# Optimization experiments

Measured on AMD Instinct MI355X. Metric: run time of the kernel, lower is better.

Reference implementation:

```python
import jax, jax.numpy as jnp
import numpy as np

H = 1024      # hidden_size
NH = 16       # num heads
HD = H // NH  # head dim
B, S = 2, 2048


def setup_inputs() -> dict:
    key = jax.random.key(0)
    ks = jax.random.split(key, 10)
    s = 1.0 / np.sqrt(H)
    return {
        "hidden_states": jax.random.normal(ks[0], (B, S, H), dtype=jnp.float32),
        "attention_mask": jax.random.randint(ks[1], (B, S), 0, 2, dtype=jnp.int32),
        "Wq": jax.random.normal(ks[2], (H, H), dtype=jnp.float32) * s,
        "bq": jnp.zeros((H,), dtype=jnp.float32),
        "Wk": jax.random.normal(ks[3], (H, H), dtype=jnp.float32) * s,
        "bk": jnp.zeros((H,), dtype=jnp.float32),
        "Wv": jax.random.normal(ks[4], (H, H), dtype=jnp.float32) * s,
        "bv": jnp.zeros((H,), dtype=jnp.float32),
        "Wo": jax.random.normal(ks[5], (H, H), dtype=jnp.float32) * s,
        "bo": jnp.zeros((H,), dtype=jnp.float32),
    }


def _heads(x):
    # [B,S,H] -> [B,NH,S,HD]
    b, s, _ = x.shape
    return x.reshape(b, s, NH, HD).transpose(0, 2, 1, 3)


def reference(hidden_states, attention_mask, Wq, bq, Wk, bk, Wv, bv, Wo, bo):
    q = _heads(hidden_states @ Wq + bq)
    k = _heads(hidden_states @ Wk + bk)
    v = _heads(hidden_states @ Wv + bv)
    scores = jnp.einsum("bhqd,bhkd->bhqk", q, k) / jnp.sqrt(jnp.float32(HD))
    mask = attention_mask.astype(scores.dtype)[:, None, None, :]  # [B,1,1,S]
    scores = scores + mask * -10000.0
    probs = jax.nn.softmax(scores, axis=-1)  # dropout is identity in eval
    ctx = jnp.einsum("bhqk,bhkd->bhqd", probs, v)
    ctx = ctx.transpose(0, 2, 1, 3).reshape(hidden_states.shape[0], hidden_states.shape[1], H)
    return ctx @ Wo + bo
```

## Files before the change

### kernel.cpp

```cpp
#include <hip/hip_runtime.h>
#include <stdint.h>
#include <stddef.h>

#define S_LEN 2048
#define BATCH 2
#define HID 1024
#define NHEADS 16
#define HDIM 64

typedef __attribute__((ext_vector_type(8))) short short8;
typedef __attribute__((ext_vector_type(4))) short short4v;
typedef __attribute__((ext_vector_type(4))) float float4v;

#define MFMA32(a, b, c) __builtin_amdgcn_mfma_f32_16x16x32_bf16((a), (b), (c), 0, 0, 0)

#if __has_builtin(__builtin_amdgcn_mfma_f32_16x16x16_bf16)
#define MFMA16(a, b, c) __builtin_amdgcn_mfma_f32_16x16x16_bf16((a), (b), (c), 0, 0, 0)
#elif __has_builtin(__builtin_amdgcn_mfma_f32_16x16x16bf16_1k)
#define MFMA16(a, b, c) __builtin_amdgcn_mfma_f32_16x16x16bf16_1k((a), (b), (c), 0, 0, 0)
#else
static __device__ __forceinline__ float4v mfma16_asm(short4v a, short4v b, float4v c) {
  asm volatile("v_mfma_f32_16x16x16_bf16 %0, %1, %2, %0" : "+v"(c) : "v"(a), "v"(b));
  return c;
}
#define MFMA16(a, b, c) mfma16_asm((a), (b), (c))
#endif

#define SCALE_L2E 0.18033688011f

__device__ __forceinline__ short f2bf(float f) {
  union { float f; uint32_t u; } v; v.f = f;
  uint32_t u = v.u;
  uint32_t r = (u + 0x7fffu + ((u >> 16) & 1u)) >> 16;
  return (short)(uint16_t)r;
}

__device__ __forceinline__ short4v pack_bf16x4(float4v v) {
  union { short4v s; uint32_t u[2]; } U;
  U.u[0] = __builtin_amdgcn_perm(__float_as_uint(v[1]) + 0x8000u,
                                 __float_as_uint(v[0]) + 0x8000u, 0x07060302u);
  U.u[1] = __builtin_amdgcn_perm(__float_as_uint(v[3]) + 0x8000u,
                                 __float_as_uint(v[2]) + 0x8000u, 0x07060302u);
  return U.s;
}

__device__ __forceinline__ void gl_lds16(const void* g, void* l) {
  __builtin_amdgcn_global_load_lds((const __attribute__((address_space(1))) void*)g,
                                   (__attribute__((address_space(3))) void*)l,
                                   16, 0, 0);
}

__global__ __launch_bounds__(256) void prep_cast(const float* __restrict__ x,
                                                 short* __restrict__ xbf) {
  int gid = blockIdx.x * 256 + threadIdx.x;
  const float4v* src = (const float4v*)x;
  float4v v = src[gid];
  short4v o;
  o[0] = f2bf(v[0]); o[1] = f2bf(v[1]); o[2] = f2bf(v[2]); o[3] = f2bf(v[3]);
  ((short4v*)xbf)[gid] = o;
}

__global__ __launch_bounds__(256) void prep_idx(const int* __restrict__ mask,
                                                short* __restrict__ maskc,
                                                short* __restrict__ cidx,
                                                int* __restrict__ nkinfo,
                                                short* __restrict__ Kc,
                                                short* __restrict__ Vtc) {
  __shared__ int sc[256];
  const int t = threadIdx.x;
  const short neg = f2bf(-14426.9504f);
  for (int b = 0; b < BATCH; b++) {
    int m[8]; int lc = 0;
    const int* mb = mask + b * S_LEN + t * 8;
#pragma unroll
    for (int j = 0; j < 8; j++) { m[j] = mb[j]; lc += (m[j] == 0); }
    sc[t] = lc;
    __syncthreads();
#pragma unroll
    for (int off = 1; off < 256; off <<= 1) {
      int u = (t >= off) ? sc[t - off] : 0;
      int v = sc[t];
      __syncthreads();
      sc[t] = u + v;
      __syncthreads();
    }
    int excl = sc[t] - lc;
    int nk = sc[255];
    int nkpad = (nk + 63) & ~63;
    if (t == 0) nkinfo[b] = nkpad;
    int run = excl;
#pragma unroll
    for (int j = 0; j < 8; j++) {
      short v;
      if (m[j] == 0) { v = (short)run; maskc[b * S_LEN + run] = 0; run++; }
      else v = (short)-1;
      cidx[b * S_LEN + t * 8 + j] = v;
    }
    for (int i = nk + t; i < S_LEN; i += 256) maskc[b * S_LEN + i] = neg;
    for (int p = t; p < NHEADS * 64; p += 256) {
      int hh = p >> 6, sp = nk + (p & 63);
      if (sp < nkpad) {
        short* dst = Kc + ((size_t)(b * NHEADS + hh) * S_LEN + sp) * HDIM;
#pragma unroll
        for (int c8 = 0; c8 < 8; c8++) *(short8*)(dst + c8 * 8) = (short8)0;
      }
    }
    for (int p = t; p < NHEADS * HDIM; p += 256) {
      int hh = p >> 6, dd = p & 63;
      short* dst = Vtc + ((size_t)(b * NHEADS + hh) * HDIM + dd) * S_LEN;
      for (int sp = nk; sp < nkpad; sp++) dst[sp] = 0;
    }
    __syncthreads();
  }
}

__global__ __launch_bounds__(256) void prep_transpose(const float* __restrict__ w0,
                                                      const float* __restrict__ w1,
                                                      const float* __restrict__ w2,
                                                      const float* __restrict__ w3,
                                                      short* __restrict__ wt) {
  __shared__ short lds[64 * 66];
  int z = blockIdx.z;
  const float* w = (z == 0) ? w0 : (z == 1) ? w1 : (z == 2) ? w2 : w3;
  short* out = wt + (size_t)z * HID * HID;
  int k0 = blockIdx.x * 64, n0 = blockIdx.y * 64;
  int lane = threadIdx.x & 63, wrp = threadIdx.x >> 6;
#pragma unroll
  for (int i = 0; i < 16; i++) {
    int rr = wrp + i * 4;
    lds[lane * 66 + rr] = f2bf(w[(size_t)(k0 + rr) * HID + n0 + lane]);
  }
  __syncthreads();
#pragma unroll
  for (int i = 0; i < 16; i++) {
    int nn = wrp + i * 4;
    out[(size_t)(n0 + nn) * HID + k0 + lane] = lds[nn * 66 + lane];
  }
}

#define VPS 136
template <int BM, int BN, bool TRANS_EP, bool DBUF>
__global__ __launch_bounds__(256) void gemm_bt(const short* __restrict__ A,
                                               const short* __restrict__ WTbase,
                                               const float* __restrict__ bq,
                                               const float* __restrict__ bk,
                                               const float* __restrict__ bv,
                                               const float* __restrict__ bo,
                                               short* __restrict__ outQ,
                                               short* __restrict__ outK,
                                               short* __restrict__ outVt,
                                               float* __restrict__ outF,
                                               const short* __restrict__ cidx,
                                               int mode_base) {
  constexpr int RI = BM / 32;
  constexpr int RJ = BN / 32;
  constexpr int TILE = BM * 128 + BN * 128;
  constexpr int LSZ1 = DBUF ? TILE * 2 : TILE;
  constexpr int LSZ = (TRANS_EP && LSZ1 < 128 * VPS * 2) ? 128 * VPS * 2 : LSZ1;
  __shared__ __align__(16) char lds[LSZ];
  const int tid = threadIdx.x;
  const int lane = tid & 63, w = tid >> 6;
  const int wm = w & 1, wn = w >> 1;
  const int quad = lane >> 4, l15 = lane & 15;
  const int mode = mode_base + blockIdx.z;
  const short* Bt = WTbase + (size_t)mode * HID * HID;
  const float* bias = (mode == 0) ? bq : (mode == 1) ? bk : (mode == 2) ? bv : bo;
  const int m0 = blockIdx.x * BM, n0 = blockIdx.y * BN;

  float4v acc[RI][RJ];
#pragma unroll
  for (int i = 0; i < RI; i++)
#pragma unroll
    for (int j = 0; j < RJ; j++) acc[i][j] = (float4v)0.0f;

  auto issue = [&](int k0, char* buf) {
#pragma unroll
    for (int inst = 0; inst < BM / 32; inst++) {
      int p = inst * 256 + tid;
      int r = p >> 3;
      int c = (p & 7) ^ (r & 7);
      gl_lds16(A + (size_t)(m0 + r) * HID + k0 + c * 8, buf + p * 16);
    }
#pragma unroll
    for (int inst = 0; inst < BN / 32; inst++) {
      int p = inst * 256 + tid;
      int r = p >> 3;
      int c = (p & 7) ^ (r & 7);
      gl_lds16(Bt + (size_t)(n0 + r) * HID + k0 + c * 8, buf + BM * 128 + p * 16);
    }
  };

  auto compute = [&](const char* buf) {
#pragma unroll
    for (int kk = 0; kk < 2; kk++) {
      short8 af[RI], bf[RJ];
#pragma unroll
      for (int i = 0; i < RI; i++) {
        int ra = wm * (BM / 2) + i * 16 + l15;
        af[i] = *(const short8*)(buf + ra * 128 + (((kk * 4 + quad) ^ (ra & 7)) * 16));
      }
#pragma unroll
      for (int j = 0; j < RJ; j++) {
        int rb = wn * (BN / 2) + j * 16 + l15;
        bf[j] = *(const short8*)(buf + BM * 128 + rb * 128 + (((kk * 4 + quad) ^ (rb & 7)) * 16));
      }
#pragma unroll
      for (int i = 0; i < RI; i++)
#pragma unroll
        for (int j = 0; j < RJ; j++)
          acc[i][j] = MFMA32(af[i], bf[j], acc[i][j]);
    }
  };

  if (DBUF) {
    constexpr int NLD = BM / 32 + BN / 32;
    issue(0, lds);
#pragma unroll 1
    for (int t = 0; t < HID / 64; t++) {
      if (t < HID / 64 - 1) {
        issue((t + 1) * 64, lds + ((t + 1) & 1) * TILE);
        asm volatile("s_waitcnt vmcnt(%0)" ::"i"(NLD) : "memory");
      } else {
        asm volatile("s_waitcnt vmcnt(0)" ::: "memory");
      }
      __builtin_amdgcn_s_barrier();
      asm volatile("" ::: "memory");
      compute(lds + (t & 1) * TILE);
      asm volatile("" ::: "memory");
      __builtin_amdgcn_s_barrier();
    }
  } else {
    for (int k0 = 0; k0 < HID; k0 += 64) {
      __syncthreads();
      issue(k0, lds);
      __syncthreads();
      compute(lds);
    }
  }

  if (TRANS_EP && mode == 2) {
    short* eb = (short*)lds;
    __syncthreads();
#pragma unroll
    for (int j = 0; j < RJ; j++) {
      int nl = wn * (BN / 2) + j * 16 + l15;
      float bsv = bias[n0 + nl];
#pragma unroll
      for (int i = 0; i < RI; i++)
#pragma unroll
        for (int r = 0; r < 4; r++) {
          int ml = wm * (BM / 2) + i * 16 + quad * 4 + r;
          eb[nl * VPS + ml] = f2bf(acc[i][j][r] + bsv);
        }
    }
    __syncthreads();
    int row = tid >> 1, half = tid & 1;
    int n = n0 + row, h = n >> 6, d = n & 63;
    int b = m0 >> 11;
    short* dsth = outVt + ((size_t)(b * NHEADS + h) * HDIM + d) * S_LEN;
    const short* src = eb + row * VPS + half * 64;
    const short* cb = cidx + b * S_LEN + (m0 & 2047) + half * 64;
#pragma unroll 8
    for (int j = 0; j < 64; j++) {
      int sp = cb[j];
      if (sp >= 0) dsth[sp] = src[j];
    }
    return;
  }

#pragma unroll
  for (int i = 0; i < RI; i++) {
#pragma unroll
    for (int j = 0; j < RJ; j++) {
      int n = n0 + wn * (BN / 2) + j * 16 + l15;
      float bsv = bias[n];
#pragma unroll
      for (int r = 0; r < 4; r++) {
        int m = m0 + wm * (BM / 2) + i * 16 + quad * 4 + r;
        float val = acc[i][j][r] + bsv;
        if (mode == 3) {
          outF[(size_t)m * HID + n] = val;
        } else {
          int b = m >> 11, s = m & 2047, h = n >> 6, d = n & 63;
          short u = f2bf((mode == 1) ? val * SCALE_L2E : val);
          if (mode == 0) {
            outQ[((size_t)(b * NHEADS + h) * S_LEN + s) * HDIM + d] = u;
          } else {
            int sp = cidx[b * S_LEN + s];
            if (sp >= 0)
              outK[((size_t)(b * NHEADS + h) * S_LEN + sp) * HDIM + d] = u;
          }
        }
      }
    }
  }
}

#define AT_DB 16384
#define AT_VOFF 8192
#define ALDS_M 32768

__device__ __forceinline__ float* buf_addr(float* base, int row, int col) {
  return base + row * 64 + ((((col >> 2) ^ (row & 15)) << 2) | (col & 3));
}

__global__ __launch_bounds__(256, 4) void attn(const short* __restrict__ Qb,
                                               const short* __restrict__ Kb,
                                               const short* __restrict__ Vt,
                                               const short* __restrict__ maskc,
                                               const int* __restrict__ nkinfo,
                                               short* __restrict__ ctx) {
  __shared__ __align__(16) char lds[36864];
  const int tid = threadIdx.x, lane = tid & 63, w = tid >> 6;
  const int quad = lane >> 4, l15 = lane & 15;
  const int qhalf = w & 1, khalf = w >> 1;
  const int h = blockIdx.y, b = blockIdx.z, bh = b * NHEADS + h;
  const short* Qh = Qb + (size_t)bh * S_LEN * HDIM;
  const short* Kh = Kb + (size_t)bh * S_LEN * HDIM;
  const short* Vh = Vt + (size_t)bh * HDIM * S_LEN;
  const short* mbase = maskc + b * S_LEN;
  const int qb0 = blockIdx.x * 64;
  const int nkp = nkinfo[b];

  auto issueKV = [&](int kb, int bufi) {
    char* base = lds + bufi * AT_DB;
#pragma unroll
    for (int inst = 0; inst < 2; inst++) {
      int p = inst * 256 + tid;
      int r = p >> 3, c = (p & 7) ^ (r & 7);
      gl_lds16(Kh + (size_t)(kb + r) * HDIM + c * 8, base + p * 16);
      gl_lds16(Vh + (size_t)r * S_LEN + kb + c * 8, base + AT_VOFF + p * 16);
    }
  };

  gl_lds16(mbase + tid * 8, lds + ALDS_M + tid * 16);
  issueKV(0, 0);

  short8 qf[2][2];
#pragma unroll
  for (int qt = 0; qt < 2; qt++)
#pragma unroll
    for (int kk = 0; kk < 2; kk++)
      qf[qt][kk] = *(const short8*)(Qh + (size_t)(qb0 + qhalf * 32 + qt * 16 + l15) * HDIM + kk * 32 + quad * 8);

  float4v o[2][4];
#pragma unroll
  for (int qt = 0; qt < 2; qt++)
#pragma unroll
    for (int nd = 0; nd < 4; nd++) o[qt][nd] = (float4v)0.0f;
  float lp[2] = {0.0f, 0.0f};

#pragma unroll 1
  for (int kb = 0; kb < nkp; kb += 64) {
    const int cur = (kb >> 6) & 1;
    const char* base = lds + cur * AT_DB;
    if (kb + 64 < nkp) {
      issueKV(kb + 64, cur ^ 1);
      asm volatile("s_waitcnt vmcnt(%0)" ::"i"(4) : "memory");
    } else {
      asm volatile("s_waitcnt vmcnt(0)" ::: "memory");
    }
    __builtin_amdgcn_s_barrier();
    asm volatile("" ::: "memory");

#pragma unroll
    for (int mt = 0; mt < 2; mt++) {
      short4v bvf[4];
      {
        int ch = khalf * 4 + mt * 2 + (quad >> 1);
        int sub = (quad & 1) * 8;
#pragma unroll
        for (int nd = 0; nd < 4; nd++) {
          int rv = nd * 16 + l15;
          bvf[nd] = *(const short4v*)(base + AT_VOFF + rv * 128 + ((ch ^ (rv & 7)) * 16) + sub);
        }
      }
      int rk = khalf * 32 + mt * 16 + l15;
      short8 ka0 = *(const short8*)(base + rk * 128 + ((quad ^ (rk & 7)) * 16));
      short8 ka1 = *(const short8*)(base + rk * 128 + (((4 + quad) ^ (rk & 7)) * 16));
      float4v mbv;
      {
        int midx = kb + khalf * 32 + mt * 16 + quad * 4;
        short4v ms = *(const short4v*)(lds + ALDS_M + midx * 2);
#pragma unroll
        for (int r = 0; r < 4; r++)
          mbv[r] = __uint_as_float(((uint32_t)(uint16_t)ms[r]) << 16);
      }
#pragma unroll
      for (int qt = 0; qt < 2; qt++) {
        float4v c = mbv;
        c = MFMA32(ka0, qf[qt][0], c);
        c = MFMA32(ka1, qf[qt][1], c);
        float4v ev;
#pragma unroll
        for (int r = 0; r < 4; r++) ev[r] = __builtin_amdgcn_exp2f(c[r]);
        lp[qt] += (ev[0] + ev[1]) + (ev[2] + ev[3]);
        short4v ap = pack_bf16x4(ev);
#pragma unroll
        for (int nd = 0; nd < 4; nd++) o[qt][nd] = MFMA16(ap, bvf[nd], o[qt][nd]);
      }
    }
    asm volatile("" ::: "memory");
    __builtin_amdgcn_s_barrier();
  }

#pragma unroll
  for (int qt = 0; qt < 2; qt++) {
    lp[qt] += __shfl_xor(lp[qt], 16, 64);
    lp[qt] += __shfl_xor(lp[qt], 32, 64);
  }
  float* lrowS = (float*)(lds + ALDS_M);
  float* bufP = (float*)(lds + qhalf * 8192);
  if (quad == 0) {
#pragma unroll
    for (int qt = 0; qt < 2; qt++) lrowS[w * 32 + qt * 16 + l15] = lp[qt];
  }
  if (khalf == 1) {
#pragma unroll
    for (int qt = 0; qt < 2; qt++)
#pragma unroll
      for (int nd = 0; nd < 4; nd++)
#pragma unroll
        for (int r = 0; r < 4; r++)
          *buf_addr(bufP, qt * 16 + quad * 4 + r, nd * 16 + l15) = o[qt][nd][r];
  }
  __syncthreads();
  if (khalf == 0) {
#pragma unroll
    for (int qt = 0; qt < 2; qt++)
#pragma unroll
      for (int nd = 0; nd < 4; nd++)
#pragma unroll
        for (int r = 0; r < 4; r++) {
          float* p = buf_addr(bufP, qt * 16 + quad * 4 + r, nd * 16 + l15);
          *p = *p + o[qt][nd][r];
        }
  }
  __syncthreads();
  int row = w * 16 + l15;
  float ls = lrowS[row] + lrowS[64 + row];
  float inv = 1.0f / ls;
  float* bufq = (float*)(lds + (row >> 5) * 8192);
  int brow = row & 31;
  short* dstp = ctx + ((size_t)(b * S_LEN + qb0 + row) * HID + h * HDIM + quad * 16);
#pragma unroll
  for (int half = 0; half < 2; half++) {
    int c0 = quad * 16 + half * 8;
    float4v x0 = *(float4v*)buf_addr(bufq, brow, c0);
    float4v x1 = *(float4v*)buf_addr(bufq, brow, c0 + 4);
    union { short8 s; short4v h[2]; } R;
    float4v s0, s1;
#pragma unroll
    for (int i = 0; i < 4; i++) { s0[i] = x0[i] * inv; s1[i] = x1[i] * inv; }
    R.h[0] = pack_bf16x4(s0);
    R.h[1] = pack_bf16x4(s1);
    *(short8*)(dstp + half * 8) = R.s;
  }
}

extern "C" void kernel_launch(void* const* d_in, const int* in_sizes, int n_in,
                              void* d_out, int out_size, void* d_ws, size_t ws_size,
                              hipStream_t stream) {
  const float* hs = (const float*)d_in[0];
  const int* mask = (const int*)d_in[1];
  const float* Wq = (const float*)d_in[2];
  const float* bq = (const float*)d_in[3];
  const float* Wk = (const float*)d_in[4];
  const float* bk = (const float*)d_in[5];
  const float* Wv = (const float*)d_in[6];
  const float* bv = (const float*)d_in[7];
  const float* Wo = (const float*)d_in[8];
  const float* bo = (const float*)d_in[9];
  float* out = (float*)d_out;
  char* ws = (char*)d_ws;

  short* XBF = (short*)(ws);
  short* CTX = (short*)(ws);
  short* WT  = (short*)(ws + (size_t)(8u << 20));
  short* QB  = (short*)(ws + (size_t)(16u << 20));
  short* KB  = (short*)(ws + (size_t)(24u << 20));
  short* VTt = (short*)(ws + (size_t)(32u << 20));
  short* MBc = (short*)(ws + (size_t)(40u << 20));
  short* CIDX = (short*)(ws + (size_t)(40u << 20) + (64u << 10));
  int*   NKI  = (int*)(ws + (size_t)(40u << 20) + (128u << 10));

  prep_cast<<<4096, 256, 0, stream>>>(hs, XBF);
  prep_idx<<<1, 256, 0, stream>>>(mask, MBc, CIDX, NKI, KB, VTt);
  prep_transpose<<<dim3(16, 16, 4), 256, 0, stream>>>(Wq, Wk, Wv, Wo, WT);
  gemm_bt<128, 128, true, true><<<dim3(32, 8, 3), 256, 0, stream>>>(XBF, WT, bq, bk, bv, bo, QB, KB, VTt, nullptr, CIDX, 0);
  attn<<<dim3(32, NHEADS, BATCH), 256, 0, stream>>>(QB, KB, VTt, MBc, NKI, CTX);
  gemm_bt<64, 128, false, true><<<dim3(64, 8, 1), 256, 0, stream>>>(CTX, WT, bq, bk, bv, bo, nullptr, nullptr, nullptr, out, nullptr, 3);
}
```

Before: 200.2 us.

## Compact unmasked rows before K/V projection and skip fully masked tiles

```diff
diff --git a/kernel.cpp b/kernel.cpp
--- a/kernel.cpp
+++ b/kernel.cpp
@@ -62,10 +62,8 @@
 
 __global__ __launch_bounds__(256) void prep_idx(const int* __restrict__ mask,
                                                 short* __restrict__ maskc,
-                                                short* __restrict__ cidx,
-                                                int* __restrict__ nkinfo,
-                                                short* __restrict__ Kc,
-                                                short* __restrict__ Vtc) {
+                                                short* __restrict__ iidx,
+                                                int* __restrict__ nkinfo) {
   __shared__ int sc[256];
   const int t = threadIdx.x;
   const short neg = f2bf(-14426.9504f);
@@ -86,31 +84,35 @@
     }
     int excl = sc[t] - lc;
     int nk = sc[255];
-    int nkpad = (nk + 63) & ~63;
-    if (t == 0) nkinfo[b] = nkpad;
+    if (t == 0) { nkinfo[b] = (nk + 63) & ~63; nkinfo[2 + b] = nk; }
     int run = excl;
 #pragma unroll
     for (int j = 0; j < 8; j++) {
-      short v;
-      if (m[j] == 0) { v = (short)run; maskc[b * S_LEN + run] = 0; run++; }
-      else v = (short)-1;
-      cidx[b * S_LEN + t * 8 + j] = v;
-    }
-    for (int i = nk + t; i < S_LEN; i += 256) maskc[b * S_LEN + i] = neg;
-    for (int p = t; p < NHEADS * 64; p += 256) {
-      int hh = p >> 6, sp = nk + (p & 63);
-      if (sp < nkpad) {
-        short* dst = Kc + ((size_t)(b * NHEADS + hh) * S_LEN + sp) * HDIM;
-#pragma unroll
-        for (int c8 = 0; c8 < 8; c8++) *(short8*)(dst + c8 * 8) = (short8)0;
-      }
-    }
-    for (int p = t; p < NHEADS * HDIM; p += 256) {
-      int hh = p >> 6, dd = p & 63;
-      short* dst = Vtc + ((size_t)(b * NHEADS + hh) * HDIM + dd) * S_LEN;
-      for (int sp = nk; sp < nkpad; sp++) dst[sp] = 0;
-    }
+      if (m[j] == 0) { iidx[b * S_LEN + run] = (short)(t * 8 + j); run++; }
+    }
+    for (int i = t; i < S_LEN; i += 256)
+      maskc[b * S_LEN + i] = (i < nk) ? (short)0 : neg;
     __syncthreads();
+  }
+}
+
+__global__ __launch_bounds__(256) void prep_compact(const short* __restrict__ xbf,
+                                                    const short* __restrict__ iidx,
+                                                    const int* __restrict__ nkinfo,
+                                                    short* __restrict__ xc) {
+  const int t = threadIdx.x;
+  const int b = blockIdx.x >> 8;
+  const int row = (blockIdx.x & 255) * 8 + (t >> 5);
+  const int ch = (t & 31) * 32;
+  const int nk = nkinfo[2 + b];
+  short* dst = xc + ((size_t)b * S_LEN + row) * HID + ch;
+  if (row < nk) {
+    const short* src = xbf + ((size_t)b * S_LEN + iidx[b * S_LEN + row]) * HID + ch;
+#pragma unroll
+    for (int k = 0; k < 4; k++) *(short8*)(dst + k * 8) = *(const short8*)(src + k * 8);
+  } else {
+#pragma unroll
+    for (int k = 0; k < 4; k++) *(short8*)(dst + k * 8) = (short8)0;
   }
 }
 
@@ -140,7 +142,8 @@
 
 #define VPS 136
 template <int BM, int BN, bool TRANS_EP, bool DBUF>
-__global__ __launch_bounds__(256) void gemm_bt(const short* __restrict__ A,
+__global__ __launch_bounds__(256) void gemm_bt(const short* __restrict__ A0,
+                                               const short* __restrict__ AC,
                                                const short* __restrict__ WTbase,
                                                const float* __restrict__ bq,
                                                const float* __restrict__ bk,
@@ -150,7 +153,7 @@
                                                short* __restrict__ outK,
                                                short* __restrict__ outVt,
                                                float* __restrict__ outF,
-                                               const short* __restrict__ cidx,
+                                               const int* __restrict__ nki,
                                                int mode_base) {
   constexpr int RI = BM / 32;
   constexpr int RJ = BN / 32;
@@ -163,9 +166,11 @@
   const int wm = w & 1, wn = w >> 1;
   const int quad = lane >> 4, l15 = lane & 15;
   const int mode = mode_base + blockIdx.z;
+  const int m0 = blockIdx.x * BM, n0 = blockIdx.y * BN;
+  if ((mode == 1 || mode == 2) && (m0 & 2047) >= nki[m0 >> 11]) return;
+  const short* A = (mode == 1 || mode == 2) ? AC : A0;
   const short* Bt = WTbase + (size_t)mode * HID * HID;
   const float* bias = (mode == 0) ? bq : (mode == 1) ? bk : (mode == 2) ? bv : bo;
-  const int m0 = blockIdx.x * BM, n0 = blockIdx.y * BN;
 
   float4v acc[RI][RJ];
 #pragma unroll
@@ -256,15 +261,12 @@
     __syncthreads();
     int row = tid >> 1, half = tid & 1;
     int n = n0 + row, h = n >> 6, d = n & 63;
-    int b = m0 >> 11;
-    short* dsth = outVt + ((size_t)(b * NHEADS + h) * HDIM + d) * S_LEN;
+    int b = m0 >> 11, sc = (m0 & 2047) + half * 64;
+    short* dst = outVt + ((size_t)(b * NHEADS + h) * HDIM + d) * S_LEN + sc;
     const short* src = eb + row * VPS + half * 64;
-    const short* cb = cidx + b * S_LEN + (m0 & 2047) + half * 64;
-#pragma unroll 8
-    for (int j = 0; j < 64; j++) {
-      int sp = cb[j];
-      if (sp >= 0) dsth[sp] = src[j];
-    }
+#pragma unroll
+    for (int c = 0; c < 8; c++)
+      *(short8*)(dst + c * 8) = *(const short8*)(src + c * 8);
     return;
   }
 
@@ -282,14 +284,12 @@
           outF[(size_t)m * HID + n] = val;
         } else {
           int b = m >> 11, s = m & 2047, h = n >> 6, d = n & 63;
-          short u = f2bf((mode == 1) ? val * SCALE_L2E : val);
-          if (mode == 0) {
+          if (mode == 1) val *= SCALE_L2E;
+          short u = f2bf(val);
+          if (mode == 0)
             outQ[((size_t)(b * NHEADS + h) * S_LEN + s) * HDIM + d] = u;
-          } else {
-            int sp = cidx[b * S_LEN + s];
-            if (sp >= 0)
-              outK[((size_t)(b * NHEADS + h) * S_LEN + sp) * HDIM + d] = u;
-          }
+          else
+            outK[((size_t)(b * NHEADS + h) * S_LEN + s) * HDIM + d] = u;
         }
       }
     }
@@ -481,13 +481,15 @@
   short* KB  = (short*)(ws + (size_t)(24u << 20));
   short* VTt = (short*)(ws + (size_t)(32u << 20));
   short* MBc = (short*)(ws + (size_t)(40u << 20));
-  short* CIDX = (short*)(ws + (size_t)(40u << 20) + (64u << 10));
+  short* IIDX = (short*)(ws + (size_t)(40u << 20) + (64u << 10));
   int*   NKI  = (int*)(ws + (size_t)(40u << 20) + (128u << 10));
+  short* XC  = (short*)(ws + (size_t)(41u << 20));
 
   prep_cast<<<4096, 256, 0, stream>>>(hs, XBF);
-  prep_idx<<<1, 256, 0, stream>>>(mask, MBc, CIDX, NKI, KB, VTt);
+  prep_idx<<<1, 256, 0, stream>>>(mask, MBc, IIDX, NKI);
+  prep_compact<<<512, 256, 0, stream>>>(XBF, IIDX, NKI, XC);
   prep_transpose<<<dim3(16, 16, 4), 256, 0, stream>>>(Wq, Wk, Wv, Wo, WT);
-  gemm_bt<128, 128, true, true><<<dim3(32, 8, 3), 256, 0, stream>>>(XBF, WT, bq, bk, bv, bo, QB, KB, VTt, nullptr, CIDX, 0);
+  gemm_bt<128, 128, true, true><<<dim3(32, 8, 3), 256, 0, stream>>>(XBF, XC, WT, bq, bk, bv, bo, QB, KB, VTt, nullptr, NKI, 0);
   attn<<<dim3(32, NHEADS, BATCH), 256, 0, stream>>>(QB, KB, VTt, MBc, NKI, CTX);
-  gemm_bt<64, 128, false, true><<<dim3(64, 8, 1), 256, 0, stream>>>(CTX, WT, bq, bk, bv, bo, nullptr, nullptr, nullptr, out, nullptr, 3);
-}
+  gemm_bt<64, 128, false, true><<<dim3(64, 8, 1), 256, 0, stream>>>(CTX, nullptr, WT, bq, bk, bv, bo, nullptr, nullptr, nullptr, out, nullptr, 3);
+}
```

After: 175.6 us. 12.3% less time.
